# Kernel optimization log

Hardware: AMD Instinct MI355X
Metric: run time of the kernel (lower is better)

Reference implementation:

```python
import jax, jax.numpy as jnp
import numpy as np

HEADS = 4
DIM_HEAD = 32
DIM = 128
HIDDEN = HEADS * DIM_HEAD  # 128


def setup_inputs() -> dict:
    key = jax.random.key(0)
    k1, k2, k3 = jax.random.split(key, 3)
    B, C, H, W = 16, DIM, 128, 128
    x = jax.random.normal(k1, (B, C, H, W), dtype=jnp.float32)
    # 1x1 convs are pointwise channel mixes: weight [out_ch, in_ch]
    w_qkv = jax.random.normal(k2, (3 * HIDDEN, C), dtype=jnp.float32) * 0.05
    w_out = jax.random.normal(k3, (DIM, HIDDEN), dtype=jnp.float32) * 0.05
    b_out = jnp.zeros((DIM,), dtype=jnp.float32)
    return {"x": x, "w_qkv": w_qkv, "w_out": w_out, "b_out": b_out}


def reference(x, w_qkv, w_out, b_out):
    b, c, H, W = x.shape
    n = H * W
    scale = DIM_HEAD ** -0.5
    # to_qkv: 1x1 conv == channel GEMM -> [b, 3*hidden, n], then split (tf.split axis=1)
    qkv = jnp.einsum('oc,bchw->bohw', w_qkv, x).reshape(b, 3, HEADS, DIM_HEAD, n)
    q, k, v = qkv[:, 0], qkv[:, 1], qkv[:, 2]  # each [b, h, d, n]
    q = q * scale
    k = jax.nn.softmax(k, axis=-1)  # softmax over spatial tokens n
    context = jnp.einsum('bhdn,bhen->bhde', k, v)   # [b, h, d, e], small d x e
    out = jnp.einsum('bhde,bhdn->bhen', context, q)  # [b, h, e, n]
    out = out.reshape(b, HIDDEN, H, W)
    # to_out: 1x1 conv with bias
    return jnp.einsum('oc,bchw->bohw', w_out, out) + b_out[None, :, None, None]
```

## Files before the change

### kernel.cpp

```cpp
#include <hip/hip_runtime.h>
#include <cmath>

#define NBATCH 16
#define NCH    128
#define NPIX   16384
#define NREP   2

#define WS_S_OFF 0
#define WS_A_OFF (NBATCH * NREP * 128)
#define WS_ZERO_FLOATS (WS_A_OFF + NBATCH * NREP * 4096)
#define WS_MBF_BYTE ((size_t)WS_ZERO_FLOATS * 4)

typedef __bf16 bf16x8 __attribute__((ext_vector_type(8)));
typedef __bf16 bf16x4 __attribute__((ext_vector_type(4)));
typedef __bf16 bf16x2 __attribute__((ext_vector_type(2)));
typedef float  f32x4  __attribute__((ext_vector_type(4)));

#define MFMA16(a, b, c) __builtin_amdgcn_mfma_f32_16x16x32_bf16((a), (b), (c), 0, 0, 0)

__global__ __launch_bounds__(256, 2) void k1_partials(const float* __restrict__ x,
                                                      const float* __restrict__ w_qkv,
                                                      float* __restrict__ ws)
{
    const int b = blockIdx.y;
    const int g = blockIdx.x;
    const int t = threadIdx.x;
    const int w = t >> 6;
    const int l = t & 63;
    const int lm = l & 15;
    const int q  = l >> 4;

    __shared__ __align__(16) __bf16 Xs[64][136];
    __shared__ __align__(16) __bf16 EVs[256][72];

    const float* wkv = w_qkv + 128 * NCH;
    bf16x8 wfrag[4][4];
#pragma unroll
    for (int rt = 0; rt < 4; ++rt) {
        const int row = (rt < 2) ? (w * 32 + rt * 16 + lm)
                                 : (128 + w * 32 + (rt - 2) * 16 + lm);
#pragma unroll
        for (int ks = 0; ks < 4; ++ks) {
            const float* src = wkv + row * NCH + ks * 32 + q * 8;
            float4 p0 = *(const float4*)src;
            float4 p1 = *(const float4*)(src + 4);
            bf16x8 f;
            f[0] = (__bf16)p0.x; f[1] = (__bf16)p0.y; f[2] = (__bf16)p0.z; f[3] = (__bf16)p0.w;
            f[4] = (__bf16)p1.x; f[5] = (__bf16)p1.y; f[6] = (__bf16)p1.z; f[7] = (__bf16)p1.w;
            wfrag[rt][ks] = f;
        }
    }

    f32x4 a_acc[2][2];
#pragma unroll
    for (int dt = 0; dt < 2; ++dt)
#pragma unroll
        for (int et = 0; et < 2; ++et) a_acc[dt][et] = (f32x4)0.f;
    float s8[8];
#pragma unroll
    for (int j = 0; j < 8; ++j) s8[j] = 0.f;

    for (int ci = 0; ci < 8; ++ci) {
        const int n0 = (g + ci * 32) * 64;

#pragma unroll
        for (int rq = 0; rq < 8; ++rq) {
            const int r0 = w * 32 + rq * 4;
            const float* xb = x + (size_t)(b * NCH + r0) * NPIX + n0 + l;
            float f0 = xb[0];
            float f1 = xb[NPIX];
            float f2 = xb[2 * NPIX];
            float f3 = xb[3 * NPIX];
            bf16x4 pk;
            pk[0] = (__bf16)f0; pk[1] = (__bf16)f1; pk[2] = (__bf16)f2; pk[3] = (__bf16)f3;
            *(bf16x4*)&Xs[l][r0] = pk;
        }
        __syncthreads();

        f32x4 acc[4][4];
#pragma unroll
        for (int rt = 0; rt < 4; ++rt)
#pragma unroll
            for (int ct = 0; ct < 4; ++ct) acc[rt][ct] = (f32x4)0.f;

#pragma unroll
        for (int ks = 0; ks < 4; ++ks) {
            bf16x8 bf[4];
#pragma unroll
            for (int ct = 0; ct < 4; ++ct)
                bf[ct] = *(const bf16x8*)&Xs[ct * 16 + lm][ks * 32 + q * 8];
#pragma unroll
            for (int rt = 0; rt < 4; ++rt)
#pragma unroll
                for (int ct = 0; ct < 4; ++ct)
                    acc[rt][ct] = MFMA16(wfrag[rt][ks], bf[ct], acc[rt][ct]);
        }

#pragma unroll
        for (int rt = 0; rt < 4; ++rt) {
            const int rowbase = (rt < 2) ? (w * 32 + rt * 16)
                                         : (128 + w * 32 + (rt - 2) * 16);
#pragma unroll
            for (int ct = 0; ct < 4; ++ct) {
                f32x4 v = acc[rt][ct];
                if (rt < 2) {
#pragma unroll
                    for (int r = 0; r < 4; ++r) {
                        float e = __expf(v[r]);
                        v[r] = e;
                        s8[rt * 4 + r] += e;
                    }
                }
                const int colw = ct * 16 + (lm & ~1);
#pragma unroll
                for (int s = 0; s < 2; ++s) {
                    float fe = v[2 * s];
                    float fo = v[2 * s + 1];
                    float ge = __shfl_xor(fe, 1);
                    float go = __shfl_xor(fo, 1);
                    bf16x2 pw;
                    if (l & 1) { pw[0] = (__bf16)go; pw[1] = (__bf16)fo; }
                    else       { pw[0] = (__bf16)fe; pw[1] = (__bf16)ge; }
                    const int roww = rowbase + q * 4 + 2 * s + (l & 1);
                    *(bf16x2*)&EVs[roww][colw] = pw;
                }
            }
        }

#pragma unroll
        for (int ks2 = 0; ks2 < 2; ++ks2) {
            bf16x8 ea[2], vb[2];
#pragma unroll
            for (int dt = 0; dt < 2; ++dt)
                ea[dt] = *(const bf16x8*)&EVs[w * 32 + dt * 16 + lm][ks2 * 32 + q * 8];
#pragma unroll
            for (int et = 0; et < 2; ++et)
                vb[et] = *(const bf16x8*)&EVs[128 + w * 32 + et * 16 + lm][ks2 * 32 + q * 8];
#pragma unroll
            for (int dt = 0; dt < 2; ++dt)
#pragma unroll
                for (int et = 0; et < 2; ++et)
                    a_acc[dt][et] = MFMA16(ea[dt], vb[et], a_acc[dt][et]);
        }
        __syncthreads();
    }

    const int rep = g & (NREP - 1);

#pragma unroll
    for (int j = 0; j < 8; ++j) {
        float v = s8[j];
        v += __shfl_xor(v, 1);
        v += __shfl_xor(v, 2);
        v += __shfl_xor(v, 4);
        v += __shfl_xor(v, 8);
        s8[j] = v;
    }
    if (lm == 0) {
        float* Sp = ws + WS_S_OFF + (size_t)(b * NREP + rep) * 128;
#pragma unroll
        for (int rt2 = 0; rt2 < 2; ++rt2)
#pragma unroll
            for (int r = 0; r < 4; ++r)
                atomicAdd(&Sp[w * 32 + rt2 * 16 + q * 4 + r], s8[rt2 * 4 + r]);
    }
    {
        float* Ab = ws + WS_A_OFF + (size_t)((b * NREP + rep) * 4 + w) * 1024;
#pragma unroll
        for (int dt = 0; dt < 2; ++dt)
#pragma unroll
            for (int et = 0; et < 2; ++et)
#pragma unroll
                for (int r = 0; r < 4; ++r)
                    atomicAdd(&Ab[(dt * 16 + q * 4 + r) * 32 + et * 16 + lm],
                              a_acc[dt][et][r]);
    }
}

__global__ __launch_bounds__(256) void k2_mprime(const float* __restrict__ w_qkv,
                                                 const float* __restrict__ w_out,
                                                 const float* __restrict__ ws,
                                                 __bf16* __restrict__ Mbf)
{
    const int b  = blockIdx.x;
    const int o0 = blockIdx.y * 32;
    const int t  = threadIdx.x;

    __shared__ float ctx[4][32][32];
    __shared__ float Ts[32][128];
    __shared__ float Wqs[32][128];
    __shared__ float Ss[128];

    if (t < 128) {
        float s = 0.f;
#pragma unroll
        for (int r = 0; r < NREP; ++r)
            s += ws[WS_S_OFF + (size_t)(b * NREP + r) * 128 + t];
        Ss[t] = s;
    }
    __syncthreads();

    for (int i = t; i < 4096; i += 256) {
        float a = 0.f;
#pragma unroll
        for (int r = 0; r < NREP; ++r)
            a += ws[WS_A_OFF + (size_t)(b * NREP + r) * 4096 + i];
        const int hh = i >> 10, d = (i >> 5) & 31, e = i & 31;
        ctx[hh][d][e] = a / Ss[hh * 32 + d];
    }
    __syncthreads();

    {
        const int oo  = t >> 3;
        const int o   = o0 + oo;
        const int hd0 = (t & 7) * 16;
        const int hh  = hd0 >> 5;
        const int db  = hd0 & 31;
        float wo[32];
#pragma unroll
        for (int e4 = 0; e4 < 32; e4 += 4)
            *(float4*)&wo[e4] = *(const float4*)&w_out[o * NCH + hh * 32 + e4];
#pragma unroll
        for (int k = 0; k < 16; ++k) {
            const int d = db + k;
            float s = 0.f;
#pragma unroll
            for (int e = 0; e < 32; ++e) s = fmaf(wo[e], ctx[hh][d][e], s);
            Ts[oo][hd0 + k] = s;
        }
    }
    __syncthreads();

    float macc[16];
#pragma unroll
    for (int ii = 0; ii < 16; ++ii) macc[ii] = 0.f;

    for (int slab = 0; slab < 4; ++slab) {
        for (int i = t; i < 32 * 128; i += 256)
            Wqs[i >> 7][i & 127] = w_qkv[(size_t)(slab * 32 + (i >> 7)) * NCH + (i & 127)];
        __syncthreads();
#pragma unroll
        for (int ii = 0; ii < 16; ++ii) {
            const int i  = t + ii * 256;
            const int oo = i >> 7;
            const int c  = i & 127;
            float s = macc[ii];
#pragma unroll
            for (int k = 0; k < 32; ++k)
                s = fmaf(Ts[oo][slab * 32 + k], Wqs[k][c], s);
            macc[ii] = s;
        }
        __syncthreads();
    }

    const float scale = 0.17677669529663687f;
#pragma unroll
    for (int ii = 0; ii < 16; ++ii) {
        const int i  = t + ii * 256;
        const int oo = i >> 7;
        const int c  = i & 127;
        Mbf[(size_t)(b * NCH + o0 + oo) * NCH + c] = (__bf16)(macc[ii] * scale);
    }
}

__global__ __launch_bounds__(256, 2) void k3_out(const float* __restrict__ x,
                                                 const float* __restrict__ bias,
                                                 const __bf16* __restrict__ Mbf,
                                                 float* __restrict__ y)
{
    const int b  = blockIdx.y;
    const int n0 = blockIdx.x * 128;
    const int t  = threadIdx.x;
    const int w  = t >> 6, l = t & 63;
    const int lm = l & 15, q = l >> 4;
    const int rw = (w & 1) * 64;
    const int pw = (w >> 1) * 64;

    __shared__ __align__(16) __bf16 Xs[128][136];

    const __bf16* Mb = Mbf + (size_t)b * NCH * NCH;
    bf16x8 mfrag[4][4];
#pragma unroll
    for (int rt = 0; rt < 4; ++rt)
#pragma unroll
        for (int ks = 0; ks < 4; ++ks)
            mfrag[rt][ks] = *(const bf16x8*)&Mb[(size_t)(rw + rt * 16 + lm) * NCH + ks * 32 + q * 8];

#pragma unroll
    for (int rq = 0; rq < 8; ++rq) {
        const int r0 = w * 32 + rq * 4;
        const float* xb = x + (size_t)(b * NCH + r0) * NPIX + n0;
        {
            float f0 = xb[l], f1 = xb[NPIX + l], f2 = xb[2 * NPIX + l], f3 = xb[3 * NPIX + l];
            bf16x4 pk;
            pk[0] = (__bf16)f0; pk[1] = (__bf16)f1; pk[2] = (__bf16)f2; pk[3] = (__bf16)f3;
            *(bf16x4*)&Xs[l][r0] = pk;
        }
        {
            float f0 = xb[64 + l], f1 = xb[NPIX + 64 + l], f2 = xb[2 * NPIX + 64 + l], f3 = xb[3 * NPIX + 64 + l];
            bf16x4 pk;
            pk[0] = (__bf16)f0; pk[1] = (__bf16)f1; pk[2] = (__bf16)f2; pk[3] = (__bf16)f3;
            *(bf16x4*)&Xs[64 + l][r0] = pk;
        }
    }
    __syncthreads();

    f32x4 acc[4][4];
#pragma unroll
    for (int rt = 0; rt < 4; ++rt)
#pragma unroll
        for (int ct = 0; ct < 4; ++ct) acc[rt][ct] = (f32x4)0.f;

#pragma unroll
    for (int ks = 0; ks < 4; ++ks) {
        bf16x8 bf[4];
#pragma unroll
        for (int ct = 0; ct < 4; ++ct)
            bf[ct] = *(const bf16x8*)&Xs[pw + ct * 16 + lm][ks * 32 + q * 8];
#pragma unroll
        for (int rt = 0; rt < 4; ++rt)
#pragma unroll
            for (int ct = 0; ct < 4; ++ct)
                acc[rt][ct] = MFMA16(mfrag[rt][ks], bf[ct], acc[rt][ct]);
    }

#pragma unroll
    for (int rt = 0; rt < 4; ++rt) {
#pragma unroll
        for (int r = 0; r < 4; ++r) {
            const int row = rw + rt * 16 + q * 4 + r;
            const float bb = bias[row];
            float* yp = y + (size_t)(b * NCH + row) * NPIX + n0 + pw + lm;
#pragma unroll
            for (int ct = 0; ct < 4; ++ct)
                yp[ct * 16] = acc[rt][ct][r] + bb;
        }
    }
}

extern "C" void kernel_launch(void* const* d_in, const int* in_sizes, int n_in,
                              void* d_out, int out_size, void* d_ws, size_t ws_size,
                              hipStream_t stream) {
    (void)in_sizes; (void)n_in; (void)out_size; (void)ws_size;
    const float* x     = (const float*)d_in[0];
    const float* w_qkv = (const float*)d_in[1];
    const float* w_out = (const float*)d_in[2];
    const float* b_out = (const float*)d_in[3];
    float*  y   = (float*)d_out;
    float*  ws  = (float*)d_ws;
    __bf16* Mbf = (__bf16*)((char*)d_ws + WS_MBF_BYTE);

    hipMemsetAsync(d_ws, 0, (size_t)WS_ZERO_FLOATS * 4, stream);

    k1_partials<<<dim3(32, NBATCH),         256, 0, stream>>>(x, w_qkv, ws);
    k2_mprime  <<<dim3(NBATCH, 4),          256, 0, stream>>>(w_qkv, w_out, ws, Mbf);
    k3_out     <<<dim3(NPIX / 128, NBATCH), 256, 0, stream>>>(x, b_out, Mbf, y);
}
```

Baseline: 324.9 us.

## Prefetch next x chunk into registers in k1, halve EV LDS, shrink k3 tiles

```diff
diff --git a/kernel.cpp b/kernel.cpp
--- a/kernel.cpp
+++ b/kernel.cpp
@@ -17,6 +17,10 @@
 typedef float  f32x4  __attribute__((ext_vector_type(4)));
 
 #define MFMA16(a, b, c) __builtin_amdgcn_mfma_f32_16x16x32_bf16((a), (b), (c), 0, 0, 0)
+
+__device__ __forceinline__ void barrier_lds() {
+    asm volatile("s_waitcnt lgkmcnt(0)\n\ts_barrier" ::: "memory");
+}
 
 __global__ __launch_bounds__(256, 2) void k1_partials(const float* __restrict__ x,
                                                       const float* __restrict__ w_qkv,
@@ -31,7 +35,7 @@
     const int q  = l >> 4;
 
     __shared__ __align__(16) __bf16 Xs[64][136];
-    __shared__ __align__(16) __bf16 EVs[256][72];
+    __shared__ __align__(16) __bf16 EVs[256][40];
 
     const float* wkv = w_qkv + 128 * NCH;
     bf16x8 wfrag[4][4];
@@ -60,22 +64,41 @@
 #pragma unroll
     for (int j = 0; j < 8; ++j) s8[j] = 0.f;
 
+    float fx[8][4];
+    const float* xbase = x + (size_t)(b * NCH + w * 32) * NPIX + l;
+
+    {
+        const int n0 = g * 64;
+#pragma unroll
+        for (int rq = 0; rq < 8; ++rq) {
+            const float* xb = xbase + (size_t)(rq * 4) * NPIX + n0;
+            fx[rq][0] = xb[0];
+            fx[rq][1] = xb[NPIX];
+            fx[rq][2] = xb[2 * NPIX];
+            fx[rq][3] = xb[3 * NPIX];
+        }
+    }
+
     for (int ci = 0; ci < 8; ++ci) {
-        const int n0 = (g + ci * 32) * 64;
-
 #pragma unroll
         for (int rq = 0; rq < 8; ++rq) {
-            const int r0 = w * 32 + rq * 4;
-            const float* xb = x + (size_t)(b * NCH + r0) * NPIX + n0 + l;
-            float f0 = xb[0];
-            float f1 = xb[NPIX];
-            float f2 = xb[2 * NPIX];
-            float f3 = xb[3 * NPIX];
             bf16x4 pk;
-            pk[0] = (__bf16)f0; pk[1] = (__bf16)f1; pk[2] = (__bf16)f2; pk[3] = (__bf16)f3;
-            *(bf16x4*)&Xs[l][r0] = pk;
-        }
-        __syncthreads();
+            pk[0] = (__bf16)fx[rq][0]; pk[1] = (__bf16)fx[rq][1];
+            pk[2] = (__bf16)fx[rq][2]; pk[3] = (__bf16)fx[rq][3];
+            *(bf16x4*)&Xs[l][w * 32 + rq * 4] = pk;
+        }
+        if (ci < 7) {
+            const int n0 = (g + (ci + 1) * 32) * 64;
+#pragma unroll
+            for (int rq = 0; rq < 8; ++rq) {
+                const float* xb = xbase + (size_t)(rq * 4) * NPIX + n0;
+                fx[rq][0] = xb[0];
+                fx[rq][1] = xb[NPIX];
+                fx[rq][2] = xb[2 * NPIX];
+                fx[rq][3] = xb[3 * NPIX];
+            }
+        }
+        barrier_lds();
 
         f32x4 acc[4][4];
 #pragma unroll
@@ -97,52 +120,54 @@
         }
 
 #pragma unroll
-        for (int rt = 0; rt < 4; ++rt) {
-            const int rowbase = (rt < 2) ? (w * 32 + rt * 16)
-                                         : (128 + w * 32 + (rt - 2) * 16);
-#pragma unroll
-            for (int ct = 0; ct < 4; ++ct) {
-                f32x4 v = acc[rt][ct];
-                if (rt < 2) {
-#pragma unroll
-                    for (int r = 0; r < 4; ++r) {
-                        float e = __expf(v[r]);
-                        v[r] = e;
-                        s8[rt * 4 + r] += e;
+        for (int hf = 0; hf < 2; ++hf) {
+#pragma unroll
+            for (int rt = 0; rt < 4; ++rt) {
+                const int rowbase = (rt < 2) ? (w * 32 + rt * 16)
+                                             : (128 + w * 32 + (rt - 2) * 16);
+#pragma unroll
+                for (int c2 = 0; c2 < 2; ++c2) {
+                    const int ct = hf * 2 + c2;
+                    f32x4 v = acc[rt][ct];
+                    if (rt < 2) {
+#pragma unroll
+                        for (int r = 0; r < 4; ++r) {
+                            float e = __expf(v[r]);
+                            v[r] = e;
+                            s8[rt * 4 + r] += e;
+                        }
+                    }
+                    const int colw = c2 * 16 + (lm & ~1);
+#pragma unroll
+                    for (int s = 0; s < 2; ++s) {
+                        float fe = v[2 * s];
+                        float fo = v[2 * s + 1];
+                        float ge = __shfl_xor(fe, 1);
+                        float go = __shfl_xor(fo, 1);
+                        bf16x2 pw;
+                        if (l & 1) { pw[0] = (__bf16)go; pw[1] = (__bf16)fo; }
+                        else       { pw[0] = (__bf16)fe; pw[1] = (__bf16)ge; }
+                        const int roww = rowbase + q * 4 + 2 * s + (l & 1);
+                        *(bf16x2*)&EVs[roww][colw] = pw;
                     }
                 }
-                const int colw = ct * 16 + (lm & ~1);
-#pragma unroll
-                for (int s = 0; s < 2; ++s) {
-                    float fe = v[2 * s];
-                    float fo = v[2 * s + 1];
-                    float ge = __shfl_xor(fe, 1);
-                    float go = __shfl_xor(fo, 1);
-                    bf16x2 pw;
-                    if (l & 1) { pw[0] = (__bf16)go; pw[1] = (__bf16)fo; }
-                    else       { pw[0] = (__bf16)fe; pw[1] = (__bf16)ge; }
-                    const int roww = rowbase + q * 4 + 2 * s + (l & 1);
-                    *(bf16x2*)&EVs[roww][colw] = pw;
-                }
             }
-        }
-
-#pragma unroll
-        for (int ks2 = 0; ks2 < 2; ++ks2) {
-            bf16x8 ea[2], vb[2];
-#pragma unroll
-            for (int dt = 0; dt < 2; ++dt)
-                ea[dt] = *(const bf16x8*)&EVs[w * 32 + dt * 16 + lm][ks2 * 32 + q * 8];
-#pragma unroll
-            for (int et = 0; et < 2; ++et)
-                vb[et] = *(const bf16x8*)&EVs[128 + w * 32 + et * 16 + lm][ks2 * 32 + q * 8];
-#pragma unroll
-            for (int dt = 0; dt < 2; ++dt)
+            {
+                bf16x8 ea[2], vb[2];
+#pragma unroll
+                for (int dt = 0; dt < 2; ++dt)
+                    ea[dt] = *(const bf16x8*)&EVs[w * 32 + dt * 16 + lm][q * 8];
 #pragma unroll
                 for (int et = 0; et < 2; ++et)
-                    a_acc[dt][et] = MFMA16(ea[dt], vb[et], a_acc[dt][et]);
-        }
-        __syncthreads();
+                    vb[et] = *(const bf16x8*)&EVs[128 + w * 32 + et * 16 + lm][q * 8];
+#pragma unroll
+                for (int dt = 0; dt < 2; ++dt)
+#pragma unroll
+                    for (int et = 0; et < 2; ++et)
+                        a_acc[dt][et] = MFMA16(ea[dt], vb[et], a_acc[dt][et]);
+            }
+        }
+        barrier_lds();
     }
 
     const int rep = g & (NREP - 1);
@@ -263,51 +288,41 @@
     }
 }
 
-__global__ __launch_bounds__(256, 2) void k3_out(const float* __restrict__ x,
+__global__ __launch_bounds__(256, 4) void k3_out(const float* __restrict__ x,
                                                  const float* __restrict__ bias,
                                                  const __bf16* __restrict__ Mbf,
                                                  float* __restrict__ y)
 {
     const int b  = blockIdx.y;
-    const int n0 = blockIdx.x * 128;
+    const int n0 = blockIdx.x * 64;
     const int t  = threadIdx.x;
     const int w  = t >> 6, l = t & 63;
     const int lm = l & 15, q = l >> 4;
-    const int rw = (w & 1) * 64;
-    const int pw = (w >> 1) * 64;
-
-    __shared__ __align__(16) __bf16 Xs[128][136];
+
+    __shared__ __align__(16) __bf16 Xs[64][136];
 
     const __bf16* Mb = Mbf + (size_t)b * NCH * NCH;
-    bf16x8 mfrag[4][4];
-#pragma unroll
-    for (int rt = 0; rt < 4; ++rt)
+    bf16x8 mfrag[2][4];
+#pragma unroll
+    for (int rt = 0; rt < 2; ++rt)
 #pragma unroll
         for (int ks = 0; ks < 4; ++ks)
-            mfrag[rt][ks] = *(const bf16x8*)&Mb[(size_t)(rw + rt * 16 + lm) * NCH + ks * 32 + q * 8];
+            mfrag[rt][ks] = *(const bf16x8*)&Mb[(size_t)(w * 32 + rt * 16 + lm) * NCH + ks * 32 + q * 8];
 
 #pragma unroll
     for (int rq = 0; rq < 8; ++rq) {
         const int r0 = w * 32 + rq * 4;
-        const float* xb = x + (size_t)(b * NCH + r0) * NPIX + n0;
-        {
-            float f0 = xb[l], f1 = xb[NPIX + l], f2 = xb[2 * NPIX + l], f3 = xb[3 * NPIX + l];
-            bf16x4 pk;
-            pk[0] = (__bf16)f0; pk[1] = (__bf16)f1; pk[2] = (__bf16)f2; pk[3] = (__bf16)f3;
-            *(bf16x4*)&Xs[l][r0] = pk;
-        }
-        {
-            float f0 = xb[64 + l], f1 = xb[NPIX + 64 + l], f2 = xb[2 * NPIX + 64 + l], f3 = xb[3 * NPIX + 64 + l];
-            bf16x4 pk;
-            pk[0] = (__bf16)f0; pk[1] = (__bf16)f1; pk[2] = (__bf16)f2; pk[3] = (__bf16)f3;
-            *(bf16x4*)&Xs[64 + l][r0] = pk;
-        }
+        const float* xb = x + (size_t)(b * NCH + r0) * NPIX + n0 + l;
+        float f0 = xb[0], f1 = xb[NPIX], f2 = xb[2 * NPIX], f3 = xb[3 * NPIX];
+        bf16x4 pk;
+        pk[0] = (__bf16)f0; pk[1] = (__bf16)f1; pk[2] = (__bf16)f2; pk[3] = (__bf16)f3;
+        *(bf16x4*)&Xs[l][r0] = pk;
     }
     __syncthreads();
 
-    f32x4 acc[4][4];
-#pragma unroll
-    for (int rt = 0; rt < 4; ++rt)
+    f32x4 acc[2][4];
+#pragma unroll
+    for (int rt = 0; rt < 2; ++rt)
 #pragma unroll
         for (int ct = 0; ct < 4; ++ct) acc[rt][ct] = (f32x4)0.f;
 
@@ -316,21 +331,21 @@
         bf16x8 bf[4];
 #pragma unroll
         for (int ct = 0; ct < 4; ++ct)
-            bf[ct] = *(const bf16x8*)&Xs[pw + ct * 16 + lm][ks * 32 + q * 8];
-#pragma unroll
-        for (int rt = 0; rt < 4; ++rt)
+            bf[ct] = *(const bf16x8*)&Xs[ct * 16 + lm][ks * 32 + q * 8];
+#pragma unroll
+        for (int rt = 0; rt < 2; ++rt)
 #pragma unroll
             for (int ct = 0; ct < 4; ++ct)
                 acc[rt][ct] = MFMA16(mfrag[rt][ks], bf[ct], acc[rt][ct]);
     }
 
 #pragma unroll
-    for (int rt = 0; rt < 4; ++rt) {
+    for (int rt = 0; rt < 2; ++rt) {
 #pragma unroll
         for (int r = 0; r < 4; ++r) {
-            const int row = rw + rt * 16 + q * 4 + r;
+            const int row = w * 32 + rt * 16 + q * 4 + r;
             const float bb = bias[row];
-            float* yp = y + (size_t)(b * NCH + row) * NPIX + n0 + pw + lm;
+            float* yp = y + (size_t)(b * NCH + row) * NPIX + n0 + lm;
 #pragma unroll
             for (int ct = 0; ct < 4; ++ct)
                 yp[ct * 16] = acc[rt][ct][r] + bb;
@@ -352,7 +367,7 @@
 
     hipMemsetAsync(d_ws, 0, (size_t)WS_ZERO_FLOATS * 4, stream);
 
-    k1_partials<<<dim3(32, NBATCH),         256, 0, stream>>>(x, w_qkv, ws);
-    k2_mprime  <<<dim3(NBATCH, 4),          256, 0, stream>>>(w_qkv, w_out, ws, Mbf);
-    k3_out     <<<dim3(NPIX / 128, NBATCH), 256, 0, stream>>>(x, b_out, Mbf, y);
-}
+    k1_partials<<<dim3(32, NBATCH),        256, 0, stream>>>(x, w_qkv, ws);
+    k2_mprime  <<<dim3(NBATCH, 4),         256, 0, stream>>>(w_qkv, w_out, ws, Mbf);
+    k3_out     <<<dim3(NPIX / 64, NBATCH), 256, 0, stream>>>(x, b_out, Mbf, y);
+}
```

Result: no change. 323.0 us (-0.6%).
